# Kernel tuning notes

Hardware: AMD Instinct MI355X
Metric: run time of the kernel (lower is better)

## Reference

```python
import jax, jax.numpy as jnp
import numpy as np

FILTER_SIZE = 4      # pooled output size (wH = wW = 4)
STRIDE = 16          # feature stride -> spatial_scale = 1/16
C = 512              # feature_dim
H = W = 22           # feature map size (352px crop / stride 16)
NI, NS = 3, 64       # images_in_sequence, sequences
KCELLS = 6           # static bound on integer cells overlapped per bin per axis


def setup_inputs() -> dict:
    key = jax.random.key(0)
    k1, k2, k3, k4 = jax.random.split(key, 4)
    feat = jax.random.normal(k1, (NI, NS, C, H, W), dtype=jnp.float32)
    # bb = (x, y, w, h) in image coords; keep boxes inside 352px image
    xy = jax.random.uniform(k2, (NI, NS, 2), minval=0.0, maxval=96.0)
    wh = jax.random.uniform(k3, (NI, NS, 2), minval=64.0, maxval=224.0)
    bb = jnp.concatenate([xy, wh], axis=-1).astype(jnp.float32)
    # conv init: normal(0, sqrt(2/(k*k*out_ch))), zero bias (as in the torch module)
    std = np.float32(np.sqrt(2.0 / (3 * 3 * C)))
    conv_w = jax.random.normal(k4, (C, C, 3, 3), dtype=jnp.float32) * std
    conv_b = jnp.zeros((C,), jnp.float32)
    return {"feat": feat, "bb": bb, "conv_w": conv_w, "conv_b": conv_b}


def _axis_weights(start, end, size):
    """Exact PrRoIPool 1D integration weights on integer grid points.
    start, end: (N, P) continuous bin boundaries in feature coords.
    Returns (N, P, size) weights s.t. integral of the piecewise-linear
    interpolant over [start, end] = sum_i w[i] * f(i)."""
    N, P = start.shape
    s0 = jnp.floor(start).astype(jnp.int32)                  # first cell
    cell = s0[..., None] + jnp.arange(KCELLS, dtype=jnp.int32)  # (N,P,K)
    cf = cell.astype(start.dtype)
    a1 = jnp.maximum(start[..., None], cf)                   # cell-bin intersection
    a2 = jnp.maximum(jnp.minimum(end[..., None], cf + 1.0), a1)
    alpha = a1 - cf
    lim = a2 - cf
    # integral of (1-t) and t over [alpha, lim]  (PrRoIPoolingMatCalculation)
    f0 = (lim - 0.5 * lim * lim) - (alpha - 0.5 * alpha * alpha)  # weight at point `cell`
    f1 = 0.5 * lim * lim - 0.5 * alpha * alpha                    # weight at `cell+1`
    idx0, idx1 = cell, cell + 1
    v0 = (idx0 >= 0) & (idx0 < size)   # out-of-bounds feature reads are 0
    v1 = (idx1 >= 0) & (idx1 < size)
    wts = jnp.concatenate([jnp.where(v0, f0, 0.0), jnp.where(v1, f1, 0.0)], -1)
    idx = jnp.concatenate([jnp.clip(idx0, 0, size - 1), jnp.clip(idx1, 0, size - 1)], -1)
    out = jnp.zeros((N, P, size), start.dtype)
    n_i = jnp.arange(N)[:, None, None]
    p_i = jnp.arange(P)[None, :, None]
    return out.at[n_i, p_i, idx].add(wts)


def prroi_pool(feat, rois, pooled, scale):
    """Precise RoI pooling. feat: (N,C,H,W); rois: (N,4) = (x1,y1,x2,y2),
    image coords; roi i pools from image i. Returns (N,C,pooled,pooled)."""
    x1, y1, x2, y2 = (rois[:, k] * scale for k in range(4))
    bin_w = (x2 - x1) / pooled
    bin_h = (y2 - y1) / pooled
    p = jnp.arange(pooled, dtype=feat.dtype)
    sh = y1[:, None] + p * bin_h[:, None]; eh = sh + bin_h[:, None]   # (N,P)
    sw = x1[:, None] + p * bin_w[:, None]; ew = sw + bin_w[:, None]
    Wy = _axis_weights(sh, eh, feat.shape[2])   # (N,P,H)
    Wx = _axis_weights(sw, ew, feat.shape[3])   # (N,P,W)
    acc = jnp.einsum('nph,nqw,nchw->ncpq', Wy, Wx, feat)
    area = jnp.maximum(bin_h * bin_w, 0.0)[:, None, None, None]
    return jnp.where(area == 0, 0.0, acc / jnp.where(area == 0, 1.0, area))


def reference(feat, bb, conv_w, conv_b):
    ni = feat.shape[0]
    x = feat.reshape(-1, C, H, W)
    x = jax.lax.conv_general_dilated(
        x, conv_w, window_strides=(1, 1), padding=((1, 1), (1, 1)),
        dimension_numbers=('NCHW', 'OIHW', 'NCHW')) + conv_b[None, :, None, None]
    b = bb.reshape(-1, 4)
    rois = jnp.concatenate([b[:, :2], b[:, :2] + b[:, 2:]], axis=-1)  # xyxy
    w = prroi_pool(x, rois, FILTER_SIZE, 1.0 / STRIDE)
    w = w.reshape(ni, -1, C, FILTER_SIZE, FILTER_SIZE).mean(axis=0)   # mean over images
    return w / (C * FILTER_SIZE * FILTER_SIZE)                        # filter_norm
```

## Files before the change

### kernel.cpp

```cpp
#include <hip/hip_runtime.h>


#define NIMG 192
#define CCH 512
#define FH 22
#define FW 22
#define SPATIAL 484
#define KDIM 4608
#define NDIM 1024
#define KQ 8
#define KSEG 576
#define CISTRIDE 1968
#define POOLBLKS 2048

typedef __bf16 bf16;
typedef __bf16 bf16x2 __attribute__((ext_vector_type(2)));
typedef __bf16 bf16x4 __attribute__((ext_vector_type(4)));
typedef __bf16 bf16x8 __attribute__((ext_vector_type(8)));
typedef float f32x2 __attribute__((ext_vector_type(2)));
typedef float f32x4 __attribute__((ext_vector_type(4)));

#define GLOBAL_AS __attribute__((address_space(1)))
#define LDS_AS __attribute__((address_space(3)))

__device__ __forceinline__ void gload_lds16(const void* g, void* l) {
  __builtin_amdgcn_global_load_lds((GLOBAL_AS const void*)g, (LDS_AS void*)l, 16, 0, 0);
}

#define LBAR()                                                   \
  do {                                                           \
    asm volatile("s_waitcnt lgkmcnt(0)" ::: "memory");           \
    __builtin_amdgcn_s_barrier();                                \
  } while (0)
#define FBAR()                                                   \
  do {                                                           \
    asm volatile("s_waitcnt vmcnt(0) lgkmcnt(0)" ::: "memory");  \
    __builtin_amdgcn_s_barrier();                                \
  } while (0)

__device__ __forceinline__ void axis_range(float a0, float aw, int& r0, int& r1) {
  const float scale = 1.f / 16.f;
  float s1 = a0 * scale;
  float s2 = (a0 + aw) * scale;
  float bl = (s2 - s1) * 0.25f;
  float endv = (s1 + 3 * bl) + bl;
  int c0 = max(0, (int)floorf(s1));
  int c1 = min(21, (int)floorf(endv) + 1);
  r0 = max(0, c0 - 1);
  r1 = min(21, c1 + 1);
}

__device__ __forceinline__ float axis_sum(float a0, float aw, int bin) {
  const float scale = 1.f / 16.f;
  float s1 = a0 * scale;
  float s2 = (a0 + aw) * scale;
  float blen = (s2 - s1) * 0.25f;
  float start = s1 + bin * blen;
  float end = start + blen;
  float inv = 1.0f / blen;
  float S = 0.f;
  int s0i = (int)floorf(start);
  for (int kk = 0; kk < 6; ++kk) {
    int cell = s0i + kk;
    float cf = (float)cell;
    float a1 = fmaxf(start, cf);
    float a2 = fmaxf(fminf(end, cf + 1.f), a1);
    float alpha = a1 - cf, lim = a2 - cf;
    float f0 = (lim - 0.5f * lim * lim) - (alpha - 0.5f * alpha * alpha);
    float f1 = 0.5f * lim * lim - 0.5f * alpha * alpha;
    if (cell >= 0 && cell < 22) S += f0 * inv;
    if (cell + 1 >= 0 && cell + 1 < 22) S += f1 * inv;
  }
  return S;
}

__global__ __launch_bounds__(256, 4) void pool_feat_kernel(
    const float* __restrict__ feat, const float* __restrict__ bb,
    const float* __restrict__ cw, bf16* __restrict__ Wb,
    bf16* __restrict__ Gb) {
  __shared__ __align__(16) char tileb[16 * CISTRIDE];
  __shared__ float wyl3[3 * 264];
  __shared__ float wxl3[3 * 264];
  int t = threadIdx.x;
  if (blockIdx.x >= POOLBLKS) {
    int co = blockIdx.x - POOLBLKS;
    float* lw = (float*)tileb;
    const float* src = cw + (long)co * CCH * 9;
    #pragma unroll
    for (int k = 0; k < 18; ++k) lw[t + 256 * k] = src[t + 256 * k];
    __syncthreads();
    bf16* dst = Wb + (long)co * 9 * CCH;
    #pragma unroll
    for (int k = 0; k < 18; ++k) {
      int f = t + 256 * k;
      int pos = f >> 9;
      int ci = f & 511;
      dst[f] = (bf16)lw[ci * 9 + pos];
    }
    return;
  }
  int s = blockIdx.x >> 5;
  int ciq = blockIdx.x & 31;
  int p = t >> 6;
  int lane = t & 63;
  int ci16 = lane & 15;
  int vq = lane >> 4;

  int yr0a[3], yr1a[3], xr0a[3], xr1a[3];
  #pragma unroll
  for (int i = 0; i < 3; ++i) {
    int n = i * 64 + s;
    axis_range(bb[n * 4 + 1], bb[n * 4 + 3], yr0a[i], yr1a[i]);
    axis_range(bb[n * 4 + 0], bb[n * 4 + 2], xr0a[i], xr1a[i]);
  }

  f32x4 A[9];
  #pragma unroll
  for (int a = 0; a < 9; ++a) A[a] = (f32x4){0.f, 0.f, 0.f, 0.f};
  const float* tf = (const float*)tileb;

  auto STAGE = [&](int img) {
    int n = img * 64 + s;
    int start16 = (yr0a[img] * 88) & ~15;
    int end16 = ((yr1a[img] + 1) * 88 + 15) & ~15;
    int cpi = (end16 - start16 + 1023) >> 10;
    const float* fpl0 = feat + ((long)n * CCH + ciq * 16) * SPATIAL;
    for (int k = p; k < 16 * cpi; k += 4) {
      int ci = (cpi == 2) ? (k >> 1) : k;
      int c = (cpi == 2) ? (k & 1) : 0;
      int cs = (c == cpi - 1) ? end16 - 1024 : start16;
      if (cs < 0) cs = 0;
      gload_lds16((const char*)(fpl0 + (long)ci * SPATIAL) + cs + lane * 16,
                  tileb + ci * CISTRIDE + cs + lane * 16);
    }
  };

  auto COMPUTE = [&](int img) {
    int yr0 = yr0a[img], yr1 = yr1a[img];
    int vbase = xr0a[img] & ~1;
    int npairs = ((xr1a[img] - vbase) >> 1) + 1;
    const float* wy = wyl3 + img * 264;
    const f32x4* wx = (const f32x4*)(wxl3 + img * 264);
    const f32x2* pl2 = (const f32x2*)(tf + ci16 * (CISTRIDE / 4));
    for (int j = vq; j < npairs; j += 4) {
      int vg = vbase + 2 * j;
      float a00 = 0.f, a01 = 0.f, a10 = 0.f, a11 = 0.f, a20 = 0.f, a21 = 0.f;
      for (int u = yr0; u <= yr1; ++u) {
        f32x2 f = pl2[(u * FW + vg) >> 1];
        float w0 = wy[u * 4 + p];
        float w1 = wy[(22 + u) * 4 + p];
        float w2 = wy[(44 + u) * 4 + p];
        a00 = fmaf(w0, f[0], a00); a01 = fmaf(w0, f[1], a01);
        a10 = fmaf(w1, f[0], a10); a11 = fmaf(w1, f[1], a11);
        a20 = fmaf(w2, f[0], a20); a21 = fmaf(w2, f[1], a21);
      }
      #pragma unroll
      for (int kx = 0; kx < 3; ++kx) {
        f32x4 wx0 = wx[kx * 22 + vg];
        f32x4 wx1 = wx[kx * 22 + vg + 1];
        A[kx] += wx0 * a00 + wx1 * a01;
        A[3 + kx] += wx0 * a10 + wx1 * a11;
        A[6 + kx] += wx0 * a20 + wx1 * a21;
      }
    }
  };

  STAGE(0);
  for (int idx = t; idx < 1584; idx += 256)
    (idx < 792 ? wyl3[idx] : wxl3[idx - 792]) = 0.f;
  LBAR();
  if (t < 24) {
    int img = t >> 3;
    int axis = (t >> 2) & 1;
    int bin = t & 3;
    int n = img * 64 + s;
    const float scale = 1.f / 16.f;
    float a0 = axis ? bb[n * 4 + 0] : bb[n * 4 + 1];
    float aw = axis ? bb[n * 4 + 2] : bb[n * 4 + 3];
    float s1 = a0 * scale;
    float s2 = (a0 + aw) * scale;
    float blen = (s2 - s1) * 0.25f;
    float start = s1 + bin * blen;
    float end = start + blen;
    float inv = 1.0f / blen;
    float* tbl = (axis ? wxl3 : wyl3) + img * 264;
    int s0i = (int)floorf(start);
    for (int kk = 0; kk < 6; ++kk) {
      int cell = s0i + kk;
      float cf = (float)cell;
      float a1 = fmaxf(start, cf);
      float a2 = fmaxf(fminf(end, cf + 1.f), a1);
      float alpha = a1 - cf, lim = a2 - cf;
      float f0 = (lim - 0.5f * lim * lim) - (alpha - 0.5f * alpha - 0.5f * alpha * alpha + 0.5f * alpha);
      f0 = (lim - 0.5f * lim * lim) - (alpha - 0.5f * alpha * alpha);
      float f1 = 0.5f * lim * lim - 0.5f * alpha * alpha;
      if (cell >= 0 && cell < 22) {
        float w = f0 * inv;
        #pragma unroll
        for (int ky = 0; ky < 3; ++ky) {
          int u = cell + ky - 1;
          if (u >= 0 && u < 22) tbl[(ky * 22 + u) * 4 + bin] += w;
        }
      }
      if (cell + 1 >= 0 && cell + 1 < 22) {
        float w = f1 * inv;
        #pragma unroll
        for (int ky = 0; ky < 3; ++ky) {
          int u = cell + ky;
          if (u >= 0 && u < 22) tbl[(ky * 22 + u) * 4 + bin] += w;
        }
      }
    }
  }
  FBAR();
  COMPUTE(0);
  #pragma unroll 1
  for (int img = 1; img < 3; ++img) {
    LBAR();
    STAGE(img);
    FBAR();
    COMPUTE(img);
  }

  #pragma unroll
  for (int pos = 0; pos < 9; ++pos) {
    #pragma unroll
    for (int q = 0; q < 4; ++q) {
      A[pos][q] += __shfl_xor(A[pos][q], 16);
      A[pos][q] += __shfl_xor(A[pos][q], 32);
    }
  }
  if (vq == 0) {
    int ci = ciq * 16 + ci16;
    #pragma unroll
    for (int pos = 0; pos < 9; ++pos)
      #pragma unroll
      for (int q = 0; q < 4; ++q)
        Gb[(long)(s * 16 + p * 4 + q) * KDIM + pos * CCH + ci] = (bf16)A[pos][q];
  }
}

__global__ __launch_bounds__(256, 2) void gemm_kernel(const bf16* __restrict__ Wb,
                                                      const bf16* __restrict__ Gb,
                                                      bf16* __restrict__ Opart) {
  __shared__ __align__(16) bf16 As[128 * 64];
  __shared__ __align__(16) bf16 Bs[64 * 64];
  int bid = blockIdx.x;
  int kq = bid & 7;
  int nt = (bid >> 3) & 15;
  int mt = bid >> 7;
  int co0 = mt << 7;
  int n0 = nt << 6;
  int kbase = kq * KSEG;

  int tid = threadIdx.x;
  int wv = tid >> 6, l = tid & 63;
  int wm = wv >> 1, wn = wv & 1;
  int lrow = l >> 3;
  int cg8 = ((l & 7) ^ lrow) << 3;

  long aOff[4], bOff[2];
  #pragma unroll
  for (int j = 0; j < 4; ++j) {
    int row = j * 32 + wv * 8 + lrow;
    aOff[j] = (long)(co0 + row) * KDIM + kbase + cg8;
  }
  #pragma unroll
  for (int j = 0; j < 2; ++j) {
    int row = j * 32 + wv * 8 + lrow;
    bOff[j] = (long)(n0 + row) * KDIM + kbase + cg8;
  }

  const f32x4 vz = {0.f, 0.f, 0.f, 0.f};
  f32x4 acc[4][2];
  #pragma unroll
  for (int a = 0; a < 4; ++a)
    #pragma unroll
    for (int b = 0; b < 2; ++b) acc[a][b] = vz;

  for (int c = 0; c < 9; ++c) {
    long sh = c * 64;
    #pragma unroll
    for (int j = 0; j < 4; ++j)
      gload_lds16(Wb + aOff[j] + sh, (char*)As + (j * 32 + wv * 8) * 128);
    #pragma unroll
    for (int j = 0; j < 2; ++j)
      gload_lds16(Gb + bOff[j] + sh, (char*)Bs + (j * 32 + wv * 8) * 128);
    __syncthreads();
    bf16x8 af[2][4], bfv[2][2];
    #pragma unroll
    for (int kk = 0; kk < 2; ++kk) {
      #pragma unroll
      for (int i = 0; i < 4; ++i) {
        int rowa = wm * 64 + i * 16 + (l & 15);
        int offa = rowa * 128 + kk * 64 + ((l >> 4) * 16);
        offa ^= (rowa & 7) << 4;
        af[kk][i] = *(const bf16x8*)((const char*)As + offa);
      }
      #pragma unroll
      for (int i = 0; i < 2; ++i) {
        int rowb = wn * 32 + i * 16 + (l & 15);
        int offb = rowb * 128 + kk * 64 + ((l >> 4) * 16);
        offb ^= (rowb & 7) << 4;
        bfv[kk][i] = *(const bf16x8*)((const char*)Bs + offb);
      }
    }
    #pragma unroll
    for (int kk = 0; kk < 2; ++kk)
      #pragma unroll
      for (int mi = 0; mi < 4; ++mi)
        #pragma unroll
        for (int nj = 0; nj < 2; ++nj)
          acc[mi][nj] = __builtin_amdgcn_mfma_f32_16x16x32_bf16(
              af[kk][mi], bfv[kk][nj], acc[mi][nj], 0, 0, 0);
    __syncthreads();
  }

  bf16* op = Opart + (long)kq * CCH * NDIM;
  #pragma unroll
  for (int nj = 0; nj < 2; ++nj) {
    int nn = n0 + wn * 32 + nj * 16 + (l & 15);
    #pragma unroll
    for (int mi = 0; mi < 4; ++mi) {
      #pragma unroll
      for (int rr = 0; rr < 4; ++rr) {
        int co = co0 + wm * 64 + mi * 16 + (l >> 4) * 4 + rr;
        op[(long)co * NDIM + nn] = (bf16)acc[mi][nj][rr];
      }
    }
  }
}

__global__ __launch_bounds__(256) void epi_kernel(const bf16* __restrict__ Opart,
                                                  const float* __restrict__ bb,
                                                  const float* __restrict__ cb,
                                                  float* __restrict__ out) {
  __shared__ float bfl[16];
  int bid = blockIdx.x;
  int t = threadIdx.x;
  int s = bid >> 3;
  if (t < 16) {
    int p = t >> 2;
    int q = t & 3;
    float acc = 0.f;
    #pragma unroll
    for (int i = 0; i < 3; ++i) {
      int n = i * 64 + s;
      acc += axis_sum(bb[n * 4 + 1], bb[n * 4 + 3], p) *
             axis_sum(bb[n * 4 + 0], bb[n * 4 + 2], q);
    }
    bfl[t] = acc;
  }
  __syncthreads();
  int base = (bid * 256 + t) * 4;
  int co = (base >> 4) & 511;
  int p = (base >> 2) & 3;
  long osrc = (long)co * NDIM + s * 16 + p * 4;
  f32x4 v = {0.f, 0.f, 0.f, 0.f};
  #pragma unroll
  for (int kq = 0; kq < KQ; ++kq) {
    bf16x4 o = *(const bf16x4*)(Opart + (long)kq * CCH * NDIM + osrc);
    #pragma unroll
    for (int j = 0; j < 4; ++j) v[j] += (float)o[j];
  }
  f32x4 bf4 = {bfl[p * 4 + 0], bfl[p * 4 + 1], bfl[p * 4 + 2], bfl[p * 4 + 3]};
  const float fin = 1.f / (3.f * 512.f * 16.f);
  v = (v + cb[co] * bf4) * fin;
  *(f32x4*)(out + base) = v;
}

extern "C" void kernel_launch(void* const* d_in, const int* in_sizes, int n_in,
                              void* d_out, int out_size, void* d_ws, size_t ws_size,
                              hipStream_t stream) {
  const float* feat = (const float*)d_in[0];
  const float* bb = (const float*)d_in[1];
  const float* cw = (const float*)d_in[2];
  const float* cb = (const float*)d_in[3];
  float* out = (float*)d_out;

  const size_t WB_BYTES = (size_t)CCH * 9 * CCH * 2;
  const size_t GB_BYTES = (size_t)NDIM * KDIM * 2;
  const size_t OP_BYTES = (size_t)KQ * CCH * NDIM * 2;
  if (ws_size < WB_BYTES + GB_BYTES + OP_BYTES) return;

  char* ws = (char*)d_ws;
  bf16* Wb = (bf16*)ws;
  bf16* Gb = (bf16*)(ws + WB_BYTES);
  bf16* Opart = (bf16*)(ws + WB_BYTES + GB_BYTES);

  hipLaunchKernelGGL(pool_feat_kernel, dim3(POOLBLKS + CCH), dim3(256), 0, stream,
                     feat, bb, cw, Wb, Gb);
  hipLaunchKernelGGL(gemm_kernel, dim3(512), dim3(256), 0, stream, Wb, Gb, Opart);
  hipLaunchKernelGGL(epi_kernel, dim3(512), dim3(256), 0, stream, Opart, bb, cb, out);
}
```

Before: 67.39 us.

## Fuse split-K reduction epilogue into GEMM via last-block atomic counter

Removes the separate epilogue kernel by having each GEMM tile's last-finishing K-split block, found through an atomic counter per output tile, sum the bf16 partials, add the bias term and write the output. Counters are zeroed by an extra block in the pooling kernel. This saves one kernel launch and lets the reduction overlap with GEMM blocks still running. In exchange it adds threadfences and an atomic per block, and the final reduction runs serially inside the last-arriving block of each tile. A redundant f0 expression was also cleaned up.

```diff
diff --git a/kernel.cpp b/kernel.cpp
--- a/kernel.cpp
+++ b/kernel.cpp
@@ -77,11 +77,15 @@
 __global__ __launch_bounds__(256, 4) void pool_feat_kernel(
     const float* __restrict__ feat, const float* __restrict__ bb,
     const float* __restrict__ cw, bf16* __restrict__ Wb,
-    bf16* __restrict__ Gb) {
+    bf16* __restrict__ Gb, int* __restrict__ counters) {
   __shared__ __align__(16) char tileb[16 * CISTRIDE];
   __shared__ float wyl3[3 * 264];
   __shared__ float wxl3[3 * 264];
   int t = threadIdx.x;
+  if (blockIdx.x == POOLBLKS + CCH) {
+    if (t < 64) counters[t] = 0;
+    return;
+  }
   if (blockIdx.x >= POOLBLKS) {
     int co = blockIdx.x - POOLBLKS;
     float* lw = (float*)tileb;
@@ -191,8 +195,7 @@
       float a1 = fmaxf(start, cf);
       float a2 = fmaxf(fminf(end, cf + 1.f), a1);
       float alpha = a1 - cf, lim = a2 - cf;
-      float f0 = (lim - 0.5f * lim * lim) - (alpha - 0.5f * alpha - 0.5f * alpha * alpha + 0.5f * alpha);
-      f0 = (lim - 0.5f * lim * lim) - (alpha - 0.5f * alpha * alpha);
+      float f0 = (lim - 0.5f * lim * lim) - (alpha - 0.5f * alpha * alpha);
       float f1 = 0.5f * lim * lim - 0.5f * alpha * alpha;
       if (cell >= 0 && cell < 22) {
         float w = f0 * inv;
@@ -240,11 +243,15 @@
   }
 }
 
-__global__ __launch_bounds__(256, 2) void gemm_kernel(const bf16* __restrict__ Wb,
-                                                      const bf16* __restrict__ Gb,
-                                                      bf16* __restrict__ Opart) {
+__global__ __launch_bounds__(256, 2) void gemm_kernel(
+    const bf16* __restrict__ Wb, const bf16* __restrict__ Gb,
+    bf16* __restrict__ Opart, int* __restrict__ counters,
+    const float* __restrict__ bb, const float* __restrict__ cb,
+    float* __restrict__ out) {
   __shared__ __align__(16) bf16 As[128 * 64];
   __shared__ __align__(16) bf16 Bs[64 * 64];
+  __shared__ int lastFlag;
+  __shared__ float bfl[64];
   int bid = blockIdx.x;
   int kq = bid & 7;
   int nt = (bid >> 3) & 15;
@@ -329,44 +336,53 @@
       }
     }
   }
-}
-
-__global__ __launch_bounds__(256) void epi_kernel(const bf16* __restrict__ Opart,
-                                                  const float* __restrict__ bb,
-                                                  const float* __restrict__ cb,
-                                                  float* __restrict__ out) {
-  __shared__ float bfl[16];
-  int bid = blockIdx.x;
-  int t = threadIdx.x;
-  int s = bid >> 3;
-  if (t < 16) {
-    int p = t >> 2;
-    int q = t & 3;
-    float acc = 0.f;
+
+  __threadfence();
+  if (tid == 0) {
+    int old = atomicAdd(&counters[mt * 16 + nt], 1);
+    lastFlag = (old == KQ - 1);
+  }
+  __syncthreads();
+  if (!lastFlag) return;
+  __threadfence();
+
+  if (tid < 64) {
+    int s = (n0 >> 4) + (tid >> 4);
+    int pq = tid & 15;
+    int pp = pq >> 2, qq = pq & 3;
+    float acc2 = 0.f;
     #pragma unroll
     for (int i = 0; i < 3; ++i) {
       int n = i * 64 + s;
-      acc += axis_sum(bb[n * 4 + 1], bb[n * 4 + 3], p) *
-             axis_sum(bb[n * 4 + 0], bb[n * 4 + 2], q);
-    }
-    bfl[t] = acc;
+      acc2 += axis_sum(bb[n * 4 + 1], bb[n * 4 + 3], pp) *
+              axis_sum(bb[n * 4 + 0], bb[n * 4 + 2], qq);
+    }
+    bfl[tid] = acc2;
   }
   __syncthreads();
-  int base = (bid * 256 + t) * 4;
-  int co = (base >> 4) & 511;
-  int p = (base >> 2) & 3;
-  long osrc = (long)co * NDIM + s * 16 + p * 4;
-  f32x4 v = {0.f, 0.f, 0.f, 0.f};
-  #pragma unroll
-  for (int kq = 0; kq < KQ; ++kq) {
-    bf16x4 o = *(const bf16x4*)(Opart + (long)kq * CCH * NDIM + osrc);
-    #pragma unroll
-    for (int j = 0; j < 4; ++j) v[j] += (float)o[j];
-  }
-  f32x4 bf4 = {bfl[p * 4 + 0], bfl[p * 4 + 1], bfl[p * 4 + 2], bfl[p * 4 + 3]};
   const float fin = 1.f / (3.f * 512.f * 16.f);
-  v = (v + cb[co] * bf4) * fin;
-  *(f32x4*)(out + base) = v;
+  #pragma unroll
+  for (int k = 0; k < 8; ++k) {
+    int idx = tid + 256 * k;
+    int co_l = idx >> 4;
+    int ng = idx & 15;
+    int co = co0 + co_l;
+    int n = n0 + ng * 4;
+    f32x4 v = {0.f, 0.f, 0.f, 0.f};
+    #pragma unroll
+    for (int kq2 = 0; kq2 < KQ; ++kq2) {
+      bf16x4 o = *(const bf16x4*)(Opart + (long)kq2 * CCH * NDIM +
+                                  (long)co * NDIM + n);
+      #pragma unroll
+      for (int j = 0; j < 4; ++j) v[j] += (float)o[j];
+    }
+    int s_l = ng >> 2;
+    int pqb = (ng & 3) * 4;
+    f32x4 bf4 = {bfl[s_l * 16 + pqb + 0], bfl[s_l * 16 + pqb + 1],
+                 bfl[s_l * 16 + pqb + 2], bfl[s_l * 16 + pqb + 3]};
+    v = (v + cb[co] * bf4) * fin;
+    *(f32x4*)(out + (long)(n >> 4) * 8192 + co * 16 + pqb) = v;
+  }
 }
 
 extern "C" void kernel_launch(void* const* d_in, const int* in_sizes, int n_in,
@@ -381,15 +397,17 @@
   const size_t WB_BYTES = (size_t)CCH * 9 * CCH * 2;
   const size_t GB_BYTES = (size_t)NDIM * KDIM * 2;
   const size_t OP_BYTES = (size_t)KQ * CCH * NDIM * 2;
-  if (ws_size < WB_BYTES + GB_BYTES + OP_BYTES) return;
+  const size_t CNT_BYTES = 64 * 4;
+  if (ws_size < WB_BYTES + GB_BYTES + OP_BYTES + CNT_BYTES) return;
 
   char* ws = (char*)d_ws;
   bf16* Wb = (bf16*)ws;
   bf16* Gb = (bf16*)(ws + WB_BYTES);
   bf16* Opart = (bf16*)(ws + WB_BYTES + GB_BYTES);
-
-  hipLaunchKernelGGL(pool_feat_kernel, dim3(POOLBLKS + CCH), dim3(256), 0, stream,
-                     feat, bb, cw, Wb, Gb);
-  hipLaunchKernelGGL(gemm_kernel, dim3(512), dim3(256), 0, stream, Wb, Gb, Opart);
-  hipLaunchKernelGGL(epi_kernel, dim3(512), dim3(256), 0, stream, Opart, bb, cb, out);
-}
+  int* counters = (int*)(ws + WB_BYTES + GB_BYTES + OP_BYTES);
+
+  hipLaunchKernelGGL(pool_feat_kernel, dim3(POOLBLKS + CCH + 1), dim3(256), 0,
+                     stream, feat, bb, cw, Wb, Gb, counters);
+  hipLaunchKernelGGL(gemm_kernel, dim3(512), dim3(256), 0, stream, Wb, Gb,
+                     Opart, counters, bb, cb, out);
+}
```

After: 137.4 us. 104% more time.
